# Optimization experiments

Hardware: AMD Instinct MI355X
Metric: run time of the kernel (lower is better)

Reference implementation:

```python
import jax, jax.numpy as jnp
import numpy as np

N = 100000      # num_nodes
E = 1600000     # num_edges
F_IN = 128      # node_feature_dim
D_IN = F_IN + 1 # +1 input_cards indicator
H = 128         # hidden dim (both layers)
NUM_CARDS = 110


def _xavier(key, shape):
    fan_out, fan_in = shape
    limit = np.sqrt(6.0 / (fan_in + fan_out))
    return jax.random.uniform(key, shape, jnp.float32, -limit, limit)


def setup_inputs() -> dict:
    key = jax.random.key(0)
    ks = jax.random.split(key, 12)
    x = jax.random.normal(ks[0], (N, F_IN), jnp.float32)
    edge_index = jax.random.randint(ks[1], (2, E), 0, N, jnp.int64)
    input_cards = jax.random.randint(ks[2], (N,), 0, 2, jnp.int32)
    # SAGEConv layer 1: lin_l (neighbors), lin_r (self), each [H, D_IN] + bias
    Wl1 = _xavier(ks[3], (H, D_IN)); bl1 = jnp.zeros((H,), jnp.float32)
    Wr1 = _xavier(ks[4], (H, D_IN)); br1 = jnp.zeros((H,), jnp.float32)
    # SAGEConv layer 2
    Wl2 = _xavier(ks[5], (H, H)); bl2 = jnp.zeros((H,), jnp.float32)
    Wr2 = _xavier(ks[6], (H, H)); br2 = jnp.zeros((H,), jnp.float32)
    # output layer: normal(0, 0.01)
    Wo = 0.01 * jax.random.normal(ks[7], (NUM_CARDS, H), jnp.float32)
    bo = jnp.zeros((NUM_CARDS,), jnp.float32)
    return {"x": x, "Wl1": Wl1, "bl1": bl1, "Wr1": Wr1, "br1": br1,
            "Wl2": Wl2, "bl2": bl2, "Wr2": Wr2, "br2": br2,
            "Wo": Wo, "bo": bo,
            "edge_index": edge_index, "input_cards": input_cards}


def _sage_conv_mean(h, src, dst, deg_inv, Wl, bl, Wr, br):
    # mean-aggregate source-node features at destination nodes
    summed = jax.ops.segment_sum(h[src], dst, num_segments=N)  # [N, d]
    mean = summed * deg_inv[:, None]
    return mean @ Wl.T + bl + h @ Wr.T + br


def reference(x, Wl1, bl1, Wr1, br1, Wl2, bl2, Wr2, br2, Wo, bo,
              edge_index, input_cards):
    src, dst = edge_index[0], edge_index[1]
    deg = jax.ops.segment_sum(jnp.ones((E,), jnp.float32), dst, num_segments=N)
    deg_inv = jnp.where(deg > 0, 1.0 / jnp.maximum(deg, 1.0), 0.0)
    h = jnp.concatenate([x, input_cards.astype(jnp.float32)[:, None]], axis=1)  # [N, D_IN]
    h = jax.nn.relu(_sage_conv_mean(h, src, dst, deg_inv, Wl1, bl1, Wr1, br1))
    h = jax.nn.relu(_sage_conv_mean(h, src, dst, deg_inv, Wl2, bl2, Wr2, br2))
    logits = h @ Wo.T + bo  # [N, NUM_CARDS]
    return logits
```

## Files before the change

kernel.cpp:

```cpp
#include <hip/hip_runtime.h>
#include <hip/hip_bf16.h>

#define N_NODES 100000
#define N_EDGES 1600000
#define HDIM    128
#define KCH     4
#define NUM_CARDS 110
#define NTILES  (N_NODES / 16)
#define GEMM_BLOCKS 1024

#define NB      196
#define MAXB    10240
#define PT      4096
#define PEPT    16

typedef __attribute__((ext_vector_type(8))) short bfrag;
typedef __attribute__((ext_vector_type(4))) float ffrag;
typedef __attribute__((ext_vector_type(2))) float f32x2;

__device__ inline unsigned short f2bf(float f) {
    __hip_bfloat16 h = __float2bfloat16(f);
    unsigned short u; __builtin_memcpy(&u, &h, 2); return u;
}
__device__ inline float bf_lo(unsigned int u) {
    unsigned int v = u << 16; float f; __builtin_memcpy(&f, &v, 4); return f;
}
__device__ inline float bf_hi(unsigned int u) {
    unsigned int v = u & 0xffff0000u; float f; __builtin_memcpy(&f, &v, 4); return f;
}


__global__ __launch_bounds__(256) void k_partition(
    const int* __restrict__ src, const int* __restrict__ dst,
    int* __restrict__ bucket_cursor, unsigned int* __restrict__ part) {
    __shared__ int hist[NB];
    __shared__ int hcur[NB];
    const int t = threadIdx.x;
    const int base = blockIdx.x * PT;
    for (int i = t; i < NB; i += 256) hist[i] = 0;
    __syncthreads();
#pragma unroll
    for (int i = 0; i < PEPT; i++) {
        int e = base + i * 256 + t;
        if (e < N_EDGES) atomicAdd(&hist[dst[e] >> 9], 1);
    }
    __syncthreads();
    for (int b = t; b < NB; b += 256) {
        int h = hist[b];
        hcur[b] = h ? atomicAdd(&bucket_cursor[b], h) : 0;
    }
    __syncthreads();
#pragma unroll
    for (int i = 0; i < PEPT; i++) {
        int e = base + i * 256 + t;
        if (e < N_EDGES) {
            int d = dst[e];
            int b = d >> 9;
            int r = atomicAdd(&hcur[b], 1);
            if (r < MAXB)
                part[(size_t)b * MAXB + r] =
                    ((unsigned int)(d & 511) << 17) | (unsigned int)src[e];
        }
    }
}

__global__ void k_scan_buckets(const int* __restrict__ bucket_cursor,
                               int* __restrict__ bucket_base) {
    __shared__ int s[256];
    int t = threadIdx.x;
    int v = (t < NB) ? min(bucket_cursor[t], MAXB) : 0;
    s[t] = v;
    __syncthreads();
    for (int off = 1; off < 256; off <<= 1) {
        int x = (t >= off) ? s[t - off] : 0;
        __syncthreads();
        s[t] += x;
        __syncthreads();
    }
    if (t < NB) bucket_base[t] = s[t] - v;
}

__global__ __launch_bounds__(256) void k_bucket(
    const unsigned int* __restrict__ part, const int* __restrict__ bucket_cursor,
    const int* __restrict__ bucket_base, int* __restrict__ row_off,
    int* __restrict__ deg, float* __restrict__ deg_inv,
    int* __restrict__ csr_src) {
    __shared__ int degl[512];
    __shared__ int offl[512];
    __shared__ int curl[512];
    __shared__ int stmp[256];
    const int t = threadIdx.x;
    const int b = blockIdx.x;
    const int n0 = b << 9;
    const int nb = min(512, N_NODES - n0);
    const int cnt = min(bucket_cursor[b], MAXB);
    const int row0 = bucket_base[b];
    const unsigned int* pb = &part[(size_t)b * MAXB];

    degl[t] = 0; degl[t + 256] = 0;
    __syncthreads();
    for (int i = t; i < cnt; i += 256)
        atomicAdd(&degl[pb[i] >> 17], 1);
    __syncthreads();
    const int a0 = degl[2 * t], a1 = degl[2 * t + 1];
    stmp[t] = a0 + a1;
    __syncthreads();
    for (int off = 1; off < 256; off <<= 1) {
        int x = (t >= off) ? stmp[t - off] : 0;
        __syncthreads();
        stmp[t] += x;
        __syncthreads();
    }
    const int excl = stmp[t] - (a0 + a1);
    offl[2 * t] = excl;          curl[2 * t] = excl;
    offl[2 * t + 1] = excl + a0; curl[2 * t + 1] = excl + a0;
    __syncthreads();
    for (int i = t; i < nb; i += 256) {
        int n = n0 + i;
        int d = degl[i];
        row_off[n] = row0 + offl[i];
        deg[n] = d;
        deg_inv[n] = (d > 0) ? 1.0f / (float)d : 0.0f;
    }
    for (int i = t; i < cnt; i += 256) {
        unsigned int pk = pb[i];
        int r = atomicAdd(&curl[pk >> 17], 1);
        csr_src[row0 + r] = (int)(pk & 0x1FFFFu);
    }
}


__global__ void k_prep_w(const float* __restrict__ Wl1, const float* __restrict__ Wr1,
                         const float* __restrict__ bl1, const float* __restrict__ br1,
                         const float* __restrict__ Wl2, const float* __restrict__ Wr2,
                         const float* __restrict__ bl2, const float* __restrict__ br2,
                         const float* __restrict__ Wo,  const float* __restrict__ bo,
                         unsigned short* __restrict__ W1, unsigned short* __restrict__ W2,
                         unsigned short* __restrict__ Wob,
                         float* __restrict__ bias1, float* __restrict__ bias2,
                         float* __restrict__ biaso, float* __restrict__ wcard1) {
    const int j = blockIdx.x;
    const int k = threadIdx.x;
    const float* s1 = (j < 128) ? &Wl1[(size_t)j * 129] : &Wr1[(size_t)(j - 128) * 129];
    W1[(size_t)j * HDIM + k] = f2bf(s1[k]);
    const float* s2 = (j < 128) ? &Wl2[(size_t)j * HDIM] : &Wr2[(size_t)(j - 128) * HDIM];
    W2[(size_t)j * HDIM + k] = f2bf(s2[k]);
    if (j < 112)
        Wob[(size_t)j * HDIM + k] = (j < NUM_CARDS) ? f2bf(Wo[(size_t)j * HDIM + k])
                                                    : (unsigned short)0;
    if (k == 0) {
        wcard1[j] = s1[HDIM];
        bias1[j] = (j < 128) ? 0.f : (bl1[j - 128] + br1[j - 128]);
        bias2[j] = (j < 128) ? 0.f : (bl2[j - 128] + br2[j - 128]);
        if (j < 112) biaso[j] = (j < NUM_CARDS) ? bo[j] : 0.f;
    }
}


__global__ __launch_bounds__(256) void k_gemm_dual(
    const unsigned short* __restrict__ Ab, const float* __restrict__ Af,
    const int* __restrict__ cards,
    const unsigned short* __restrict__ W,
    const float* __restrict__ bias, const float* __restrict__ wcard,
    unsigned char* __restrict__ Gq, unsigned short* __restrict__ Rb,
    int layer1) {
    const int wave = threadIdx.x >> 6;
    const int lane = threadIdx.x & 63;
    const int m16 = lane & 15;
    const int quad = lane >> 4;
    const int u0 = wave * 4;
    const bool isG = (wave < 2);

    bfrag wf[4][KCH];
    float bs[4][4], wc[4][4];
#pragma unroll
    for (int u = 0; u < 4; u++) {
        const int j = (u0 + u) * 16 + m16;
#pragma unroll
        for (int c = 0; c < KCH; c++)
            wf[u][c] = *(const bfrag*)&W[(size_t)j * HDIM + c * 32 + quad * 8];
#pragma unroll
        for (int r = 0; r < 4; r++) {
            const int jj = (u0 + u) * 16 + quad * 4 + r;
            bs[u][r] = bias[jj];
            wc[u][r] = layer1 ? wcard[jj] : 0.f;
        }
    }

    for (int tile = blockIdx.x; tile < NTILES; tile += GEMM_BLOCKS) {
        const int node = tile * 16 + m16;
        bfrag hf[KCH];
        float cv = 0.f;
        if (layer1) {
#pragma unroll
            for (int c = 0; c < KCH; c++) {
                const float4 p0 = *(const float4*)&Af[(size_t)node * HDIM + c * 32 + quad * 8];
                const float4 p1 = *(const float4*)&Af[(size_t)node * HDIM + c * 32 + quad * 8 + 4];
                bfrag h;
                h[0] = (short)f2bf(p0.x); h[1] = (short)f2bf(p0.y);
                h[2] = (short)f2bf(p0.z); h[3] = (short)f2bf(p0.w);
                h[4] = (short)f2bf(p1.x); h[5] = (short)f2bf(p1.y);
                h[6] = (short)f2bf(p1.z); h[7] = (short)f2bf(p1.w);
                hf[c] = h;
            }
            cv = (float)cards[node];
        } else {
#pragma unroll
            for (int c = 0; c < KCH; c++)
                hf[c] = *(const bfrag*)&Ab[(size_t)node * HDIM + c * 32 + quad * 8];
        }
#pragma unroll
        for (int u = 0; u < 4; u++) {
            ffrag acc = {0.f, 0.f, 0.f, 0.f};
#pragma unroll
            for (int c = 0; c < KCH; c++)
                acc = __builtin_amdgcn_mfma_f32_16x16x32_bf16(wf[u][c], hf[c], acc, 0, 0, 0);
            float v[4];
#pragma unroll
            for (int r = 0; r < 4; r++)
                v[r] = acc[r] + bs[u][r] + cv * wc[u][r];
            if (isG) {
                int pk = __builtin_amdgcn_cvt_pk_fp8_f32(v[0], v[1], 0, false);
                pk = __builtin_amdgcn_cvt_pk_fp8_f32(v[2], v[3], pk, true);
                *(unsigned int*)&Gq[(size_t)node * HDIM + (u0 + u) * 16 + quad * 4] =
                    (unsigned int)pk;
            } else {
                unsigned short o[4];
#pragma unroll
                for (int r = 0; r < 4; r++) o[r] = f2bf(v[r]);
                uint2 p = {(unsigned int)o[0] | ((unsigned int)o[1] << 16),
                           (unsigned int)o[2] | ((unsigned int)o[3] << 16)};
                *(uint2*)&Rb[(size_t)node * HDIM + (u0 + u - 8) * 16 + quad * 4] = p;
            }
        }
    }
}


__global__ __launch_bounds__(256) void k_agg(
    const unsigned char* __restrict__ Gq, const unsigned short* __restrict__ Rb,
    const int* __restrict__ row_off, const int* __restrict__ deg,
    const float* __restrict__ deg_inv, const int* __restrict__ csr_src,
    unsigned short* __restrict__ outH) {
    const int wave = threadIdx.x >> 6;
    const int lane = threadIdx.x & 63;
    const int n = blockIdx.x * 4 + wave;
    const int g = lane >> 3;
    const int l = lane & 7;
    const int start = row_off[n];
    const int d = deg[n];
    const int fo = l * 16;

    int myidx = (lane < d) ? csr_src[start + lane] : 0;

    float acc[16];
#pragma unroll
    for (int i = 0; i < 16; i++) acc[i] = 0.f;

    for (int j0 = 0; j0 < d; j0 += 8) {
        const int jj = j0 + g;
        const int asrc = __shfl(myidx, jj & 63, 64);
        uint4 gv = {0u, 0u, 0u, 0u};
        if (jj < d) {
            const int a = (jj < 64) ? asrc : csr_src[start + jj];
            gv = *(const uint4*)&Gq[(size_t)a * HDIM + fo];
        }
        const f32x2 d0 = __builtin_amdgcn_cvt_pk_f32_fp8((int)gv.x, false);
        const f32x2 d1 = __builtin_amdgcn_cvt_pk_f32_fp8((int)gv.x, true);
        const f32x2 d2 = __builtin_amdgcn_cvt_pk_f32_fp8((int)gv.y, false);
        const f32x2 d3 = __builtin_amdgcn_cvt_pk_f32_fp8((int)gv.y, true);
        const f32x2 d4 = __builtin_amdgcn_cvt_pk_f32_fp8((int)gv.z, false);
        const f32x2 d5 = __builtin_amdgcn_cvt_pk_f32_fp8((int)gv.z, true);
        const f32x2 d6 = __builtin_amdgcn_cvt_pk_f32_fp8((int)gv.w, false);
        const f32x2 d7 = __builtin_amdgcn_cvt_pk_f32_fp8((int)gv.w, true);
        acc[0] += d0.x;  acc[1] += d0.y;  acc[2] += d1.x;  acc[3] += d1.y;
        acc[4] += d2.x;  acc[5] += d2.y;  acc[6] += d3.x;  acc[7] += d3.y;
        acc[8] += d4.x;  acc[9] += d4.y;  acc[10] += d5.x; acc[11] += d5.y;
        acc[12] += d6.x; acc[13] += d6.y; acc[14] += d7.x; acc[15] += d7.y;
    }
#pragma unroll
    for (int i = 0; i < 16; i++) {
        float v = acc[i];
        v += __shfl_xor(v, 8, 64);
        v += __shfl_xor(v, 16, 64);
        v += __shfl_xor(v, 32, 64);
        acc[i] = v;
    }
    if (g == 0) {
        const float di = deg_inv[n];
        const uint4 rv0 = *(const uint4*)&Rb[(size_t)n * HDIM + fo];
        const uint4 rv1 = *(const uint4*)&Rb[(size_t)n * HDIM + fo + 8];
        const float r[16] = {bf_lo(rv0.x), bf_hi(rv0.x), bf_lo(rv0.y), bf_hi(rv0.y),
                             bf_lo(rv0.z), bf_hi(rv0.z), bf_lo(rv0.w), bf_hi(rv0.w),
                             bf_lo(rv1.x), bf_hi(rv1.x), bf_lo(rv1.y), bf_hi(rv1.y),
                             bf_lo(rv1.z), bf_hi(rv1.z), bf_lo(rv1.w), bf_hi(rv1.w)};
        unsigned short o[16];
#pragma unroll
        for (int i = 0; i < 16; i++)
            o[i] = f2bf(fmaxf(acc[i] * di + r[i], 0.f));
        uint4 p0, p1;
        p0.x = (unsigned int)o[0] | ((unsigned int)o[1] << 16);
        p0.y = (unsigned int)o[2] | ((unsigned int)o[3] << 16);
        p0.z = (unsigned int)o[4] | ((unsigned int)o[5] << 16);
        p0.w = (unsigned int)o[6] | ((unsigned int)o[7] << 16);
        p1.x = (unsigned int)o[8] | ((unsigned int)o[9] << 16);
        p1.y = (unsigned int)o[10] | ((unsigned int)o[11] << 16);
        p1.z = (unsigned int)o[12] | ((unsigned int)o[13] << 16);
        p1.w = (unsigned int)o[14] | ((unsigned int)o[15] << 16);
        *(uint4*)&outH[(size_t)n * HDIM + fo] = p0;
        *(uint4*)&outH[(size_t)n * HDIM + fo + 8] = p1;
    }
}


__global__ __launch_bounds__(256) void k_gemm_logits(
    const unsigned short* __restrict__ A, const unsigned short* __restrict__ W,
    const float* __restrict__ bias, float* __restrict__ out) {
    const int wave = threadIdx.x >> 6;
    const int lane = threadIdx.x & 63;
    const int m16 = lane & 15;
    const int quad = lane >> 4;
    const int u0 = wave * 2;

    bfrag wf[2][KCH];
    float bsj[2];
#pragma unroll
    for (int u = 0; u < 2; u++) {
        const int unit = u0 + u;
        const int j = (unit < 7 ? unit : 0) * 16 + m16;
#pragma unroll
        for (int c = 0; c < KCH; c++)
            wf[u][c] = *(const bfrag*)&W[(size_t)j * HDIM + c * 32 + quad * 8];
        bsj[u] = bias[j];
    }

    for (int tile = blockIdx.x; tile < NTILES; tile += GEMM_BLOCKS) {
        const int nodef = tile * 16 + m16;
        bfrag hf[KCH];
#pragma unroll
        for (int c = 0; c < KCH; c++)
            hf[c] = *(const bfrag*)&A[(size_t)nodef * HDIM + c * 32 + quad * 8];
#pragma unroll
        for (int u = 0; u < 2; u++) {
            const int unit = u0 + u;
            if (unit >= 7) break;
            ffrag acc = {0.f, 0.f, 0.f, 0.f};
#pragma unroll
            for (int c = 0; c < KCH; c++)
                acc = __builtin_amdgcn_mfma_f32_16x16x32_bf16(hf[c], wf[u][c], acc, 0, 0, 0);
            const int j = unit * 16 + m16;
            if (j < NUM_CARDS) {
#pragma unroll
                for (int r = 0; r < 4; r++) {
                    const int node = tile * 16 + quad * 4 + r;
                    out[(size_t)node * NUM_CARDS + j] = acc[r] + bsj[u];
                }
            }
        }
    }
}


static inline size_t align_up(size_t x, size_t a) { return (x + a - 1) & ~(a - 1); }

extern "C" void kernel_launch(void* const* d_in, const int* in_sizes, int n_in,
                              void* d_out, int out_size, void* d_ws, size_t ws_size,
                              hipStream_t stream) {
    const float* x   = (const float*)d_in[0];
    const float* Wl1 = (const float*)d_in[1];
    const float* bl1 = (const float*)d_in[2];
    const float* Wr1 = (const float*)d_in[3];
    const float* br1 = (const float*)d_in[4];
    const float* Wl2 = (const float*)d_in[5];
    const float* bl2 = (const float*)d_in[6];
    const float* Wr2 = (const float*)d_in[7];
    const float* br2 = (const float*)d_in[8];
    const float* Wo  = (const float*)d_in[9];
    const float* bo  = (const float*)d_in[10];
    const int* edge  = (const int*)d_in[11];
    const int* cards = (const int*)d_in[12];
    float* logits = (float*)d_out;

    const int* e_src = edge;
    const int* e_dst = edge + N_EDGES;

    char* w = (char*)d_ws;
    size_t off = 0;
    int* bucket_cursor = (int*)(w + off); off = align_up(off + 256 * 4, 512);
    int* bucket_base   = (int*)(w + off); off = align_up(off + 256 * 4, 512);
    unsigned int* part = (unsigned int*)(w + off); off = align_up(off + (size_t)NB * MAXB * 4, 512);
    int* row_off = (int*)(w + off); off = align_up(off + N_NODES * 4, 512);
    int* deg_i   = (int*)(w + off); off = align_up(off + N_NODES * 4, 512);
    float* dinv  = (float*)(w + off); off = align_up(off + N_NODES * 4, 512);
    int* csr_src = (int*)(w + off); off = align_up(off + (size_t)N_EDGES * 4, 512);
    unsigned char*  Gq   = (unsigned char*)(w + off);  off = align_up(off + (size_t)N_NODES * HDIM, 512);
    unsigned short* Rb   = (unsigned short*)(w + off); off = align_up(off + (size_t)N_NODES * HDIM * 2, 512);
    unsigned short* bufH = (unsigned short*)(w + off); off = align_up(off + (size_t)N_NODES * HDIM * 2, 512);
    unsigned short* W1   = (unsigned short*)(w + off); off = align_up(off + 256 * HDIM * 2, 512);
    unsigned short* W2   = (unsigned short*)(w + off); off = align_up(off + 256 * HDIM * 2, 512);
    unsigned short* Wob  = (unsigned short*)(w + off); off = align_up(off + 112 * HDIM * 2, 512);
    float* bias1  = (float*)(w + off); off = align_up(off + 256 * 4, 512);
    float* bias2  = (float*)(w + off); off = align_up(off + 256 * 4, 512);
    float* biaso  = (float*)(w + off); off = align_up(off + 112 * 4, 512);
    float* wcard1 = (float*)(w + off); off = align_up(off + 256 * 4, 512);
    (void)ws_size; (void)n_in; (void)in_sizes; (void)out_size;

    hipMemsetAsync(bucket_cursor, 0, 256 * 4, stream);
    k_prep_w<<<256, 128, 0, stream>>>(Wl1, Wr1, bl1, br1, Wl2, Wr2, bl2, br2, Wo, bo,
                                      W1, W2, Wob, bias1, bias2, biaso, wcard1);

    const int PBLK = (N_EDGES + PT - 1) / PT;
    k_partition<<<PBLK, 256, 0, stream>>>(e_src, e_dst, bucket_cursor, part);
    k_scan_buckets<<<1, 256, 0, stream>>>(bucket_cursor, bucket_base);
    k_bucket<<<NB, 256, 0, stream>>>(part, bucket_cursor, bucket_base,
                                     row_off, deg_i, dinv, csr_src);

    k_gemm_dual<<<GEMM_BLOCKS, 256, 0, stream>>>(nullptr, x, cards, W1, bias1, wcard1, Gq, Rb, 1);
    k_agg<<<N_NODES / 4, 256, 0, stream>>>(Gq, Rb, row_off, deg_i, dinv, csr_src, bufH);
    k_gemm_dual<<<GEMM_BLOCKS, 256, 0, stream>>>(bufH, nullptr, nullptr, W2, bias2, wcard1, Gq, Rb, 0);
    k_agg<<<N_NODES / 4, 256, 0, stream>>>(Gq, Rb, row_off, deg_i, dinv, csr_src, bufH);
    k_gemm_logits<<<GEMM_BLOCKS, 256, 0, stream>>>(bufH, Wob, biaso, logits);
}
```

Before: 376.6 us.

## Drop bucket scan kernel, use padded CSR, software-pipeline gather in aggregation

Removes the single-block bucket scan kernel by giving each bucket a fixed MAXB-sized slot in the CSR source array, so row offsets come from b*MAXB and one serial launch disappears. The aggregation kernel now double-buffers its gathers, issuing the next neighbour row load before converting the current one. It also precomputes byte offsets, hoists the residual load ahead of the loop, and uses packed f32x2 accumulation. The padded CSR uses more workspace and spreads edges over a sparser array.

```diff
diff --git a/kernel.cpp b/kernel.cpp
--- a/kernel.cpp
+++ b/kernel.cpp
@@ -64,26 +64,9 @@
     }
 }
 
-__global__ void k_scan_buckets(const int* __restrict__ bucket_cursor,
-                               int* __restrict__ bucket_base) {
-    __shared__ int s[256];
-    int t = threadIdx.x;
-    int v = (t < NB) ? min(bucket_cursor[t], MAXB) : 0;
-    s[t] = v;
-    __syncthreads();
-    for (int off = 1; off < 256; off <<= 1) {
-        int x = (t >= off) ? s[t - off] : 0;
-        __syncthreads();
-        s[t] += x;
-        __syncthreads();
-    }
-    if (t < NB) bucket_base[t] = s[t] - v;
-}
-
 __global__ __launch_bounds__(256) void k_bucket(
     const unsigned int* __restrict__ part, const int* __restrict__ bucket_cursor,
-    const int* __restrict__ bucket_base, int* __restrict__ row_off,
-    int* __restrict__ deg, float* __restrict__ deg_inv,
+    int* __restrict__ row_off, int* __restrict__ deg, float* __restrict__ deg_inv,
     int* __restrict__ csr_src) {
     __shared__ int degl[512];
     __shared__ int offl[512];
@@ -94,7 +77,7 @@
     const int n0 = b << 9;
     const int nb = min(512, N_NODES - n0);
     const int cnt = min(bucket_cursor[b], MAXB);
-    const int row0 = bucket_base[b];
+    const int row0 = b * MAXB;
     const unsigned int* pb = &part[(size_t)b * MAXB];
 
     degl[t] = 0; degl[t + 256] = 0;
@@ -251,53 +234,74 @@
     const int d = deg[n];
     const int fo = l * 16;
 
-    int myidx = (lane < d) ? csr_src[start + lane] : 0;
-
-    float acc[16];
-#pragma unroll
-    for (int i = 0; i < 16; i++) acc[i] = 0.f;
-
-    for (int j0 = 0; j0 < d; j0 += 8) {
-        const int jj = j0 + g;
-        const int asrc = __shfl(myidx, jj & 63, 64);
-        uint4 gv = {0u, 0u, 0u, 0u};
+    int myoff = 0;
+    if (lane < d) myoff = csr_src[start + lane] * HDIM;
+
+    uint4 rv0 = {0u, 0u, 0u, 0u}, rv1 = {0u, 0u, 0u, 0u};
+    if (g == 0) {
+        rv0 = *(const uint4*)&Rb[(size_t)n * HDIM + l * 16];
+        rv1 = *(const uint4*)&Rb[(size_t)n * HDIM + l * 16 + 8];
+    }
+
+    f32x2 acc2[8];
+#pragma unroll
+    for (int i = 0; i < 8; i++) acc2[i] = (f32x2){0.f, 0.f};
+
+    const int iters = (d + 7) >> 3;
+
+    uint4 cur = {0u, 0u, 0u, 0u};
+    {
+        const int off0 = __shfl(myoff, g, 64);
+        if (g < d) cur = *(const uint4*)&Gq[(size_t)(unsigned)off0 + fo];
+    }
+    for (int i = 1; i < iters; i++) {
+        const int jj = i * 8 + g;
+        const int offn = __shfl(myoff, jj & 63, 64);
+        uint4 nxt = {0u, 0u, 0u, 0u};
         if (jj < d) {
-            const int a = (jj < 64) ? asrc : csr_src[start + jj];
-            gv = *(const uint4*)&Gq[(size_t)a * HDIM + fo];
-        }
-        const f32x2 d0 = __builtin_amdgcn_cvt_pk_f32_fp8((int)gv.x, false);
-        const f32x2 d1 = __builtin_amdgcn_cvt_pk_f32_fp8((int)gv.x, true);
-        const f32x2 d2 = __builtin_amdgcn_cvt_pk_f32_fp8((int)gv.y, false);
-        const f32x2 d3 = __builtin_amdgcn_cvt_pk_f32_fp8((int)gv.y, true);
-        const f32x2 d4 = __builtin_amdgcn_cvt_pk_f32_fp8((int)gv.z, false);
-        const f32x2 d5 = __builtin_amdgcn_cvt_pk_f32_fp8((int)gv.z, true);
-        const f32x2 d6 = __builtin_amdgcn_cvt_pk_f32_fp8((int)gv.w, false);
-        const f32x2 d7 = __builtin_amdgcn_cvt_pk_f32_fp8((int)gv.w, true);
-        acc[0] += d0.x;  acc[1] += d0.y;  acc[2] += d1.x;  acc[3] += d1.y;
-        acc[4] += d2.x;  acc[5] += d2.y;  acc[6] += d3.x;  acc[7] += d3.y;
-        acc[8] += d4.x;  acc[9] += d4.y;  acc[10] += d5.x; acc[11] += d5.y;
-        acc[12] += d6.x; acc[13] += d6.y; acc[14] += d7.x; acc[15] += d7.y;
-    }
-#pragma unroll
-    for (int i = 0; i < 16; i++) {
-        float v = acc[i];
-        v += __shfl_xor(v, 8, 64);
-        v += __shfl_xor(v, 16, 64);
-        v += __shfl_xor(v, 32, 64);
-        acc[i] = v;
+            const int o = (jj < 64) ? offn : csr_src[start + jj] * HDIM;
+            nxt = *(const uint4*)&Gq[(size_t)(unsigned)o + fo];
+        }
+        acc2[0] += __builtin_amdgcn_cvt_pk_f32_fp8((int)cur.x, false);
+        acc2[1] += __builtin_amdgcn_cvt_pk_f32_fp8((int)cur.x, true);
+        acc2[2] += __builtin_amdgcn_cvt_pk_f32_fp8((int)cur.y, false);
+        acc2[3] += __builtin_amdgcn_cvt_pk_f32_fp8((int)cur.y, true);
+        acc2[4] += __builtin_amdgcn_cvt_pk_f32_fp8((int)cur.z, false);
+        acc2[5] += __builtin_amdgcn_cvt_pk_f32_fp8((int)cur.z, true);
+        acc2[6] += __builtin_amdgcn_cvt_pk_f32_fp8((int)cur.w, false);
+        acc2[7] += __builtin_amdgcn_cvt_pk_f32_fp8((int)cur.w, true);
+        cur = nxt;
+    }
+    acc2[0] += __builtin_amdgcn_cvt_pk_f32_fp8((int)cur.x, false);
+    acc2[1] += __builtin_amdgcn_cvt_pk_f32_fp8((int)cur.x, true);
+    acc2[2] += __builtin_amdgcn_cvt_pk_f32_fp8((int)cur.y, false);
+    acc2[3] += __builtin_amdgcn_cvt_pk_f32_fp8((int)cur.y, true);
+    acc2[4] += __builtin_amdgcn_cvt_pk_f32_fp8((int)cur.z, false);
+    acc2[5] += __builtin_amdgcn_cvt_pk_f32_fp8((int)cur.z, true);
+    acc2[6] += __builtin_amdgcn_cvt_pk_f32_fp8((int)cur.w, false);
+    acc2[7] += __builtin_amdgcn_cvt_pk_f32_fp8((int)cur.w, true);
+
+#pragma unroll
+    for (int i = 0; i < 8; i++) {
+        f32x2 v = acc2[i];
+        f32x2 t;
+        t.x = __shfl_xor(v.x, 8, 64);  t.y = __shfl_xor(v.y, 8, 64);  v += t;
+        t.x = __shfl_xor(v.x, 16, 64); t.y = __shfl_xor(v.y, 16, 64); v += t;
+        t.x = __shfl_xor(v.x, 32, 64); t.y = __shfl_xor(v.y, 32, 64); v += t;
+        acc2[i] = v;
     }
     if (g == 0) {
         const float di = deg_inv[n];
-        const uint4 rv0 = *(const uint4*)&Rb[(size_t)n * HDIM + fo];
-        const uint4 rv1 = *(const uint4*)&Rb[(size_t)n * HDIM + fo + 8];
         const float r[16] = {bf_lo(rv0.x), bf_hi(rv0.x), bf_lo(rv0.y), bf_hi(rv0.y),
                              bf_lo(rv0.z), bf_hi(rv0.z), bf_lo(rv0.w), bf_hi(rv0.w),
                              bf_lo(rv1.x), bf_hi(rv1.x), bf_lo(rv1.y), bf_hi(rv1.y),
                              bf_lo(rv1.z), bf_hi(rv1.z), bf_lo(rv1.w), bf_hi(rv1.w)};
         unsigned short o[16];
 #pragma unroll
-        for (int i = 0; i < 16; i++)
-            o[i] = f2bf(fmaxf(acc[i] * di + r[i], 0.f));
+        for (int i = 0; i < 8; i++) {
+            o[2 * i]     = f2bf(fmaxf(acc2[i].x * di + r[2 * i], 0.f));
+            o[2 * i + 1] = f2bf(fmaxf(acc2[i].y * di + r[2 * i + 1], 0.f));
+        }
         uint4 p0, p1;
         p0.x = (unsigned int)o[0] | ((unsigned int)o[1] << 16);
         p0.y = (unsigned int)o[2] | ((unsigned int)o[3] << 16);
@@ -307,8 +311,8 @@
         p1.y = (unsigned int)o[10] | ((unsigned int)o[11] << 16);
         p1.z = (unsigned int)o[12] | ((unsigned int)o[13] << 16);
         p1.w = (unsigned int)o[14] | ((unsigned int)o[15] << 16);
-        *(uint4*)&outH[(size_t)n * HDIM + fo] = p0;
-        *(uint4*)&outH[(size_t)n * HDIM + fo + 8] = p1;
+        *(uint4*)&outH[(size_t)n * HDIM + l * 16] = p0;
+        *(uint4*)&outH[(size_t)n * HDIM + l * 16 + 8] = p1;
     }
 }
 
@@ -387,12 +391,11 @@
     char* w = (char*)d_ws;
     size_t off = 0;
     int* bucket_cursor = (int*)(w + off); off = align_up(off + 256 * 4, 512);
-    int* bucket_base   = (int*)(w + off); off = align_up(off + 256 * 4, 512);
     unsigned int* part = (unsigned int*)(w + off); off = align_up(off + (size_t)NB * MAXB * 4, 512);
     int* row_off = (int*)(w + off); off = align_up(off + N_NODES * 4, 512);
     int* deg_i   = (int*)(w + off); off = align_up(off + N_NODES * 4, 512);
     float* dinv  = (float*)(w + off); off = align_up(off + N_NODES * 4, 512);
-    int* csr_src = (int*)(w + off); off = align_up(off + (size_t)N_EDGES * 4, 512);
+    int* csr_src = (int*)(w + off); off = align_up(off + (size_t)NB * MAXB * 4, 512);
     unsigned char*  Gq   = (unsigned char*)(w + off);  off = align_up(off + (size_t)N_NODES * HDIM, 512);
     unsigned short* Rb   = (unsigned short*)(w + off); off = align_up(off + (size_t)N_NODES * HDIM * 2, 512);
     unsigned short* bufH = (unsigned short*)(w + off); off = align_up(off + (size_t)N_NODES * HDIM * 2, 512);
@@ -411,8 +414,7 @@
 
     const int PBLK = (N_EDGES + PT - 1) / PT;
     k_partition<<<PBLK, 256, 0, stream>>>(e_src, e_dst, bucket_cursor, part);
-    k_scan_buckets<<<1, 256, 0, stream>>>(bucket_cursor, bucket_base);
-    k_bucket<<<NB, 256, 0, stream>>>(part, bucket_cursor, bucket_base,
+    k_bucket<<<NB, 256, 0, stream>>>(part, bucket_cursor,
                                      row_off, deg_i, dinv, csr_src);
 
     k_gemm_dual<<<GEMM_BLOCKS, 256, 0, stream>>>(nullptr, x, cards, W1, bias1, wcard1, Gq, Rb, 1);
```

After: 370.0 us. No clear change (-1.8%).
